# Optimization experiments

Hardware: AMD Instinct MI355X
Metric: run time of the kernel (lower is better)

The kernel has to match this reference:

```python
import jax, jax.numpy as jnp
import numpy as np

NM2ANG = 10.0                      # openmm_unit2model_unit_position (nm -> angstrom)
KJ2KCAL = 0.2390057361376673       # model_unit2openmm_unit_energy (kJ/mol -> kcal/mol)
CUTOFF = 5.0                       # radius-graph cutoff in model units (angstrom)
BOX_NM = 6.0                       # simulation box edge in nm
EPS = 1e-12


def setup_inputs() -> dict:
    key = jax.random.key(0)
    k1, k2, k3, k4, k5 = jax.random.split(key, 5)
    N, D, H, T = 8192, 128, 256, 100
    positions = jax.random.uniform(k1, (N, 3), dtype=jnp.float32) * BOX_NM  # nm
    node_types = jax.random.randint(k2, (N,), 0, T)                          # atomic numbers
    emb = jax.random.normal(k3, (T, D), dtype=jnp.float32)
    W1 = jax.random.normal(k4, (2 * D, H), dtype=jnp.float32) / np.sqrt(2.0 * D).astype(np.float32)
    w2 = jax.random.normal(k5, (H,), dtype=jnp.float32) / np.sqrt(float(H)).astype(np.float32)
    return {"positions": positions, "node_types": node_types, "emb": emb, "W1": W1, "w2": w2}


def reference(positions, node_types, emb, W1, w2):
    # unit scaling: openmm nm -> model angstrom
    pos = NM2ANG * positions                               # [N,3]
    # dense cdist (update_edge_index): d2 = |xi|^2 + |xj|^2 - 2 xi.xj
    sq = jnp.sum(pos * pos, axis=-1)                       # [N]
    d2 = sq[:, None] + sq[None, :] - 2.0 * (pos @ pos.T)   # [N,N]
    d = jnp.sqrt(jnp.where(d2 > EPS, d2, EPS))             # safe sqrt (diag excluded by mask)
    # radius-graph mask: (dist > 0) & (dist <= cutoff); center/neighbour filters are all-True
    mask = (d2 > EPS) & (d <= CUTOFF)                      # [N,N] bool
    # GNN energy model: distance-weighted message passing over the masked graph
    phi = jnp.where(mask, jnp.exp(-d), 0.0)                # [N,N] edge weights
    h = emb[node_types]                                    # [N,D] node embeddings
    agg = phi @ h                                          # [N,D] neighbor aggregation
    feat = jnp.concatenate([h, agg], axis=-1)              # [N,2D]
    e_node = jax.nn.relu(feat @ W1) @ w2                   # [N] per-node energy
    energy = jnp.sum(e_node)                               # scalar, kJ/mol
    return energy * KJ2KCAL                                # -> kcal/mol
```

## Files before the change

### kernel.cpp

```cpp
#include <hip/hip_runtime.h>

#define NATOMS 8192
#define DD 128
#define HH 256
#define TI 4
#define MAXE 128
#define MB 16
#define MTH 512

__global__ void k_zero(float* out) { if (threadIdx.x == 0) out[0] = 0.0f; }

__global__ __launch_bounds__(256) void k_agg(const float* __restrict__ pos,
                                             const int* __restrict__ types,
                                             const float* __restrict__ emb,
                                             float* __restrict__ agg) {
  __shared__ float sw[TI][MAXE];
  __shared__ int   srow[TI][MAXE];
  __shared__ int   scnt[TI];
  const int tid = threadIdx.x;
  const int i0 = blockIdx.x * TI;
  if (tid < TI) scnt[tid] = 0;

  float pix[TI], piy[TI], piz[TI];
#pragma unroll
  for (int m = 0; m < TI; ++m) {
    pix[m] = 10.0f * pos[(i0 + m) * 3 + 0];
    piy[m] = 10.0f * pos[(i0 + m) * 3 + 1];
    piz[m] = 10.0f * pos[(i0 + m) * 3 + 2];
  }
  __syncthreads();

  for (int j = tid; j < NATOMS; j += 256) {
    float pjx = 10.0f * pos[j * 3 + 0];
    float pjy = 10.0f * pos[j * 3 + 1];
    float pjz = 10.0f * pos[j * 3 + 2];
#pragma unroll
    for (int m = 0; m < TI; ++m) {
      float dx = pix[m] - pjx, dy = piy[m] - pjy, dz = piz[m] - pjz;
      float d2 = dx * dx;
      d2 = fmaf(dy, dy, d2);
      d2 = fmaf(dz, dz, d2);
      if (d2 > 1e-12f && d2 <= 25.0f) {
        float w = __expf(-sqrtf(d2));
        int e = atomicAdd(&scnt[m], 1);
        if (e < MAXE) {
          sw[m][e] = w;
          srow[m][e] = types[j] * DD;
        }
      }
    }
  }
  __syncthreads();

  const int d = tid & (DD - 1);
  const int g = tid >> 7;
#pragma unroll
  for (int mm = 0; mm < TI; mm += 2) {
    int m = g + mm;
    int nc = min(scnt[m], MAXE);
    float a = 0.0f;
    for (int e = 0; e < nc; ++e)
      a = fmaf(sw[m][e], emb[srow[m][e] + d], a);
    agg[(size_t)(i0 + m) * DD + d] = a;
  }
}

__global__ __launch_bounds__(MTH) void k_mlp(const int* __restrict__ types,
                                             const float* __restrict__ emb,
                                             const float* __restrict__ agg,
                                             const float* __restrict__ W1,
                                             const float* __restrict__ w2,
                                             float* __restrict__ out) {
  __shared__ float sf[2 * DD][MB];
  __shared__ float sred[MTH / 64];
  const int tid = threadIdx.x;
  const int n0 = blockIdx.x * MB;

  for (int idx = tid; idx < MB * 2 * DD; idx += MTH) {
    int j = idx >> 4;
    int m = idx & (MB - 1);
    float v;
    if (j < DD) v = emb[types[n0 + m] * DD + j];
    else        v = agg[(size_t)(n0 + m) * DD + (j - DD)];
    sf[j][m] = v;
  }
  __syncthreads();

  const int tx = tid & 127;
  const int ty = tid >> 7;
  float acc0[4], acc1[4];
#pragma unroll
  for (int m = 0; m < 4; ++m) { acc0[m] = 0.0f; acc1[m] = 0.0f; }

  const float* fbase = &sf[0][ty * 4];
#pragma unroll 4
  for (int j = 0; j < 2 * DD; ++j) {
    float w0 = W1[j * HH + tx];
    float w1 = W1[j * HH + tx + 128];
    float f[4];
    *(float4*)&f[0] = *(const float4*)(fbase + j * MB);
#pragma unroll
    for (int m = 0; m < 4; ++m) {
      acc0[m] = fmaf(f[m], w0, acc0[m]);
      acc1[m] = fmaf(f[m], w1, acc1[m]);
    }
  }

  float s0 = 0.0f, s1 = 0.0f;
#pragma unroll
  for (int m = 0; m < 4; ++m) {
    s0 += fmaxf(acc0[m], 0.0f);
    s1 += fmaxf(acc1[m], 0.0f);
  }
  float p = s0 * w2[tx] + s1 * w2[tx + 128];
#pragma unroll
  for (int off = 32; off; off >>= 1) p += __shfl_down(p, off);
  if ((tid & 63) == 0) sred[tid >> 6] = p;
  __syncthreads();
  if (tid == 0) {
    float t = 0.0f;
#pragma unroll
    for (int q = 0; q < MTH / 64; ++q) t += sred[q];
    atomicAdd(out, t * 0.2390057361376673f);
  }
}

extern "C" void kernel_launch(void* const* d_in, const int* in_sizes, int n_in,
                              void* d_out, int out_size, void* d_ws, size_t ws_size,
                              hipStream_t stream) {
  const float* pos = (const float*)d_in[0];
  const int*   typ = (const int*)d_in[1];
  const float* emb = (const float*)d_in[2];
  const float* W1  = (const float*)d_in[3];
  const float* w2  = (const float*)d_in[4];
  float* out = (float*)d_out;
  float* agg = (float*)d_ws;

  hipLaunchKernelGGL(k_zero, dim3(1), dim3(64), 0, stream, out);
  hipLaunchKernelGGL(k_agg, dim3(NATOMS / TI), dim3(256), 0, stream,
                     pos, typ, emb, agg);
  hipLaunchKernelGGL(k_mlp, dim3(NATOMS / MB), dim3(MTH), 0, stream,
                     typ, emb, agg, W1, w2, out);
}
```

Before: 119.5 us.

## Retile MLP kernel to 4x4 register tile with vectorized loads and larger node block

The MLP kernel now processes 32 nodes per block instead of 16. Each thread computes a 4-node by 4-hidden-unit register tile using float4 loads of W1 and of the shared features, replacing the previous 4x2 scalar-weight tiling. The shared-memory fill is vectorized with float4 global loads, and the launch bounds request two blocks per CU. The goal is less W1 global traffic per FMA and higher arithmetic intensity, at the cost of more registers and half as many blocks.

```diff
diff --git a/kernel.cpp b/kernel.cpp
--- a/kernel.cpp
+++ b/kernel.cpp
@@ -5,7 +5,7 @@
 #define HH 256
 #define TI 4
 #define MAXE 128
-#define MB 16
+#define MB 32
 #define MTH 512
 
 __global__ void k_zero(float* out) { if (threadIdx.x == 0) out[0] = 0.0f; }
@@ -65,54 +65,68 @@
   }
 }
 
-__global__ __launch_bounds__(MTH) void k_mlp(const int* __restrict__ types,
-                                             const float* __restrict__ emb,
-                                             const float* __restrict__ agg,
-                                             const float* __restrict__ W1,
-                                             const float* __restrict__ w2,
-                                             float* __restrict__ out) {
+__global__ __launch_bounds__(MTH, 2) void k_mlp(const int* __restrict__ types,
+                                                const float* __restrict__ emb,
+                                                const float* __restrict__ agg,
+                                                const float* __restrict__ W1,
+                                                const float* __restrict__ w2,
+                                                float* __restrict__ out) {
   __shared__ float sf[2 * DD][MB];
   __shared__ float sred[MTH / 64];
   const int tid = threadIdx.x;
   const int n0 = blockIdx.x * MB;
 
-  for (int idx = tid; idx < MB * 2 * DD; idx += MTH) {
-    int j = idx >> 4;
-    int m = idx & (MB - 1);
-    float v;
-    if (j < DD) v = emb[types[n0 + m] * DD + j];
-    else        v = agg[(size_t)(n0 + m) * DD + (j - DD)];
-    sf[j][m] = v;
+  {
+    const int m = tid & 31;
+    const int node = n0 + m;
+    const int jb0 = tid >> 5;
+    const int trow = types[node] * DD;
+#pragma unroll
+    for (int k = 0; k < 4; ++k) {
+      int jb = jb0 + 16 * k;
+      float4 v;
+      if (jb < 32) v = *(const float4*)&emb[trow + 4 * jb];
+      else         v = *(const float4*)&agg[(size_t)node * DD + 4 * (jb - 32)];
+      int j0 = 4 * jb;
+      sf[j0 + 0][m] = v.x;
+      sf[j0 + 1][m] = v.y;
+      sf[j0 + 2][m] = v.z;
+      sf[j0 + 3][m] = v.w;
+    }
   }
   __syncthreads();
 
-  const int tx = tid & 127;
-  const int ty = tid >> 7;
-  float acc0[4], acc1[4];
+  const int tx = tid & 63;
+  const int my = tid >> 6;
+  float acc[4][4];
 #pragma unroll
-  for (int m = 0; m < 4; ++m) { acc0[m] = 0.0f; acc1[m] = 0.0f; }
+  for (int r = 0; r < 4; ++r)
+#pragma unroll
+    for (int q = 0; q < 4; ++q) acc[r][q] = 0.0f;
 
-  const float* fbase = &sf[0][ty * 4];
+  const float* fb = &sf[0][4 * my];
+  const float* wp = &W1[4 * tx];
 #pragma unroll 4
   for (int j = 0; j < 2 * DD; ++j) {
-    float w0 = W1[j * HH + tx];
-    float w1 = W1[j * HH + tx + 128];
-    float f[4];
-    *(float4*)&f[0] = *(const float4*)(fbase + j * MB);
+    float w[4], f[4];
+    *(float4*)&w[0] = *(const float4*)(wp + j * HH);
+    *(float4*)&f[0] = *(const float4*)(fb + j * MB);
 #pragma unroll
-    for (int m = 0; m < 4; ++m) {
-      acc0[m] = fmaf(f[m], w0, acc0[m]);
-      acc1[m] = fmaf(f[m], w1, acc1[m]);
-    }
+    for (int r = 0; r < 4; ++r)
+#pragma unroll
+      for (int q = 0; q < 4; ++q)
+        acc[r][q] = fmaf(f[r], w[q], acc[r][q]);
   }
 
-  float s0 = 0.0f, s1 = 0.0f;
+  float wq[4];
+  *(float4*)&wq[0] = *(const float4*)&w2[4 * tx];
+  float p = 0.0f;
 #pragma unroll
-  for (int m = 0; m < 4; ++m) {
-    s0 += fmaxf(acc0[m], 0.0f);
-    s1 += fmaxf(acc1[m], 0.0f);
-  }
-  float p = s0 * w2[tx] + s1 * w2[tx + 128];
+  for (int r = 0; r < 4; ++r)
+#pragma unroll
+    for (int q = 0; q < 4; ++q)
+      p += fmaxf(acc[r][q], 0.0f) * wq[q];
+
 #pragma unroll
   for (int off = 32; off; off >>= 1) p += __shfl_down(p, off);
   if ((tid & 63) == 0) sred[tid >> 6] = p;
```

Result: faster. 116.9 us (-2.2%).

## Use bf16 MFMA for node MLP with pre-transposed bf16 weights

Applied to the files above, without the earlier changes.

Rewrites the per-node MLP as a bf16 matrix-core GEMM using 16x16x32 MFMA instructions. A prep kernel converts W1 to a transposed bf16 copy and zeroes the output, and the aggregation kernel now stores its result as bf16 to halve traffic. The FP32 FMA loop goes away, at the cost of bf16 rounding error in the energy sum.

```diff
diff --git a/kernel.cpp b/kernel.cpp
--- a/kernel.cpp
+++ b/kernel.cpp
@@ -5,15 +5,33 @@
 #define HH 256
 #define TI 4
 #define MAXE 128
-#define MB 16
-#define MTH 512
+#define BM 32
+#define KJ2KCAL 0.2390057361376673f
 
-__global__ void k_zero(float* out) { if (threadIdx.x == 0) out[0] = 0.0f; }
+typedef __attribute__((ext_vector_type(8))) short bf16x8;
+typedef __attribute__((ext_vector_type(4))) float f32x4;
+
+__device__ inline unsigned short f2bf(float x) {
+  unsigned int b = __builtin_bit_cast(unsigned int, x);
+  b += 0x7FFFu + ((b >> 16) & 1u);
+  return (unsigned short)(b >> 16);
+}
+
+__global__ void k_prep(const float* __restrict__ W1, unsigned short* __restrict__ W1bfT,
+                       float* __restrict__ out) {
+  if (blockIdx.x == 0 && threadIdx.x == 0) out[0] = 0.0f;
+  int t = blockIdx.x * 256 + threadIdx.x;
+  int n = t & 255;
+  int kb = (t >> 8) * 4;
+#pragma unroll
+  for (int i = 0; i < 4; ++i)
+    W1bfT[n * HH + kb + i] = f2bf(W1[(kb + i) * HH + n]);
+}
 
 __global__ __launch_bounds__(256) void k_agg(const float* __restrict__ pos,
                                              const int* __restrict__ types,
                                              const float* __restrict__ emb,
-                                             float* __restrict__ agg) {
+                                             unsigned short* __restrict__ aggbf) {
   __shared__ float sw[TI][MAXE];
   __shared__ int   srow[TI][MAXE];
   __shared__ int   scnt[TI];
@@ -61,67 +79,76 @@
     float a = 0.0f;
     for (int e = 0; e < nc; ++e)
       a = fmaf(sw[m][e], emb[srow[m][e] + d], a);
-    agg[(size_t)(i0 + m) * DD + d] = a;
+    aggbf[(size_t)(i0 + m) * DD + d] = f2bf(a);
   }
 }
 
-__global__ __launch_bounds__(MTH) void k_mlp(const int* __restrict__ types,
-                                             const float* __restrict__ emb,
-                                             const float* __restrict__ agg,
-                                             const float* __restrict__ W1,
-                                             const float* __restrict__ w2,
-                                             float* __restrict__ out) {
-  __shared__ float sf[2 * DD][MB];
-  __shared__ float sred[MTH / 64];
+__global__ __launch_bounds__(512, 2) void k_mlp(const int* __restrict__ types,
+                                                const float* __restrict__ emb,
+                                                const unsigned short* __restrict__ aggbf,
+                                                const unsigned short* __restrict__ W1bfT,
+                                                const float* __restrict__ w2,
+                                                float* __restrict__ out) {
+  __shared__ unsigned short sA[BM][264];
+  __shared__ float sred[8];
   const int tid = threadIdx.x;
-  const int n0 = blockIdx.x * MB;
+  const int n0 = blockIdx.x * BM;
 
-  for (int idx = tid; idx < MB * 2 * DD; idx += MTH) {
-    int j = idx >> 4;
-    int m = idx & (MB - 1);
-    float v;
-    if (j < DD) v = emb[types[n0 + m] * DD + j];
-    else        v = agg[(size_t)(n0 + m) * DD + (j - DD)];
-    sf[j][m] = v;
+  for (int idx = tid; idx < BM * 64; idx += 512) {
+    int row = idx >> 6;
+    int cb = idx & 63;
+    int node = n0 + row;
+    ushort4 u;
+    if (cb < 32) {
+      float4 v = *(const float4*)&emb[types[node] * DD + 4 * cb];
+      u.x = f2bf(v.x); u.y = f2bf(v.y); u.z = f2bf(v.z); u.w = f2bf(v.w);
+    } else {
+      u = *(const ushort4*)&aggbf[(size_t)node * DD + 4 * (cb - 32)];
+    }
+    *(ushort4*)&sA[row][4 * cb] = u;
   }
   __syncthreads();
 
-  const int tx = tid & 127;
-  const int ty = tid >> 7;
-  float acc0[4], acc1[4];
+  const int lane = tid & 63;
+  const int wv = tid >> 6;
+  const int nb = wv * 32;
+  const int l15 = lane & 15;
+  const int g = lane >> 4;
+  f32x4 acc00 = {}, acc01 = {}, acc10 = {}, acc11 = {};
+
+  const unsigned short* bp0 = W1bfT + (nb + l15) * HH + 8 * g;
+  const unsigned short* bp1 = bp0 + 16 * HH;
 #pragma unroll
-  for (int m = 0; m < 4; ++m) { acc0[m] = 0.0f; acc1[m] = 0.0f; }
-
-  const float* fbase = &sf[0][ty * 4];
-#pragma unroll 4
-  for (int j = 0; j < 2 * DD; ++j) {
-    float w0 = W1[j * HH + tx];
-    float w1 = W1[j * HH + tx + 128];
-    float f[4];
-    *(float4*)&f[0] = *(const float4*)(fbase + j * MB);
-#pragma unroll
-    for (int m = 0; m < 4; ++m) {
-      acc0[m] = fmaf(f[m], w0, acc0[m]);
-      acc1[m] = fmaf(f[m], w1, acc1[m]);
-    }
+  for (int ks = 0; ks < 8; ++ks) {
+    bf16x8 a0 = *(const bf16x8*)&sA[l15][ks * 32 + 8 * g];
+    bf16x8 a1 = *(const bf16x8*)&sA[16 + l15][ks * 32 + 8 * g];
+    bf16x8 b0 = *(const bf16x8*)(bp0 + ks * 32);
+    bf16x8 b1 = *(const bf16x8*)(bp1 + ks * 32);
+    acc00 = __builtin_amdgcn_mfma_f32_16x16x32_bf16(a0, b0, acc00, 0, 0, 0);
+    acc01 = __builtin_amdgcn_mfma_f32_16x16x32_bf16(a0, b1, acc01, 0, 0, 0);
+    acc10 = __builtin_amdgcn_mfma_f32_16x16x32_bf16(a1, b0, acc10, 0, 0, 0);
+    acc11 = __builtin_amdgcn_mfma_f32_16x16x32_bf16(a1, b1, acc11, 0, 0, 0);
   }
 
-  float s0 = 0.0f, s1 = 0.0f;
+  const float w2a = w2[nb + l15];
+  const float w2b = w2[nb + 16 + l15];
+  float p = 0.0f;
 #pragma unroll
-  for (int m = 0; m < 4; ++m) {
-    s0 += fmaxf(acc0[m], 0.0f);
-    s1 += fmaxf(acc1[m], 0.0f);
+  for (int i = 0; i < 4; ++i) {
+    p += fmaxf(acc00[i], 0.0f) * w2a;
+    p += fmaxf(acc10[i], 0.0f) * w2a;
+    p += fmaxf(acc01[i], 0.0f) * w2b;
+    p += fmaxf(acc11[i], 0.0f) * w2b;
   }
-  float p = s0 * w2[tx] + s1 * w2[tx + 128];
 #pragma unroll
   for (int off = 32; off; off >>= 1) p += __shfl_down(p, off);
-  if ((tid & 63) == 0) sred[tid >> 6] = p;
+  if (lane == 0) sred[wv] = p;
   __syncthreads();
   if (tid == 0) {
     float t = 0.0f;
 #pragma unroll
-    for (int q = 0; q < MTH / 64; ++q) t += sred[q];
-    atomicAdd(out, t * 0.2390057361376673f);
+    for (int q = 0; q < 8; ++q) t += sred[q];
+    atomicAdd(out, t * KJ2KCAL);
   }
 }
 
@@ -134,11 +161,12 @@
   const float* W1  = (const float*)d_in[3];
   const float* w2  = (const float*)d_in[4];
   float* out = (float*)d_out;
-  float* agg = (float*)d_ws;
+  unsigned short* aggbf = (unsigned short*)d_ws;
+  unsigned short* W1bfT = (unsigned short*)((char*)d_ws + NATOMS * DD * 2);
 
-  hipLaunchKernelGGL(k_zero, dim3(1), dim3(64), 0, stream, out);
+  hipLaunchKernelGGL(k_prep, dim3(64), dim3(256), 0, stream, W1, W1bfT, out);
   hipLaunchKernelGGL(k_agg, dim3(NATOMS / TI), dim3(256), 0, stream,
-                     pos, typ, emb, agg);
-  hipLaunchKernelGGL(k_mlp, dim3(NATOMS / MB), dim3(MTH), 0, stream,
-                     typ, emb, agg, W1, w2, out);
+                     pos, typ, emb, aggbf);
+  hipLaunchKernelGGL(k_mlp, dim3(NATOMS / BM), dim3(512), 0, stream,
+                     typ, emb, aggbf, W1bfT, w2, out);
 }
```

Result: faster. 100.2 us (-16.2%).
